# Kernel tuning notes

Hardware: AMD Instinct MI355X
Metric: run time of the kernel (lower is better)

Reference implementation:

```python
import jax, jax.numpy as jnp
import numpy as np

V, R, A, C, T = 50000, 5, 8, 32, 32  # vertices, radial, angular, in-channels, templates
DELTA = 2                             # rotation_delta -> n_rotations = A // DELTA = 4


def setup_inputs() -> dict:
    key = jax.random.key(0)
    ks = jax.random.split(key, 6)
    signal = jax.random.normal(ks[0], (V, C), jnp.float32)
    bc_idx = jax.random.randint(ks[1], (V, R, A, 3), 0, V, dtype=jnp.int32)
    w = jax.random.uniform(ks[2], (V, R, A, 3), jnp.float32)
    bc_w = w / jnp.sum(w, axis=-1, keepdims=True)  # barycentric weights sum to 1
    templ1 = jax.random.normal(ks[3], (T, R, A, C), jnp.float32) * 0.05
    bias1 = jnp.zeros((T,), jnp.float32)
    templ2 = jax.random.normal(ks[4], (T, R, A, T), jnp.float32) * 0.05
    bias2 = jnp.zeros((T,), jnp.float32)
    return {"signal": signal, "bc_idx": bc_idx, "bc_w": bc_w,
            "templ1": templ1, "bias1": bias1, "templ2": templ2, "bias2": bias2}


def _conv_dirac(x, bc_idx, bc_w, templ, bias):
    """Dirac intrinsic surface convolution.
    x: [V, Cin]; bc_idx/bc_w: [V, R, A, 3]; templ: [T, R, A, Cin] -> [V, n_rot, T]."""
    # Barycentric interpolation of the mesh signal at template vertices.
    gathered = x[bc_idx]                                   # [V, R, A, 3, Cin]
    interp = jnp.einsum('vrai,vraic->vrac', bc_w, gathered)  # [V, R, A, Cin]
    n_rot = A // DELTA
    # Rotating the patch by +s angular steps == correlating with templ rolled by +s.
    rot_t = jnp.stack([jnp.roll(templ, r * DELTA, axis=2) for r in range(n_rot)])  # [n_rot, T, R, A, Cin]
    return jnp.einsum('vrac,ntrac->vnt', interp, rot_t) + bias  # [V, n_rot, T]


def _amp(x):
    # AngularMaxPooling: max over the rotation axis.
    return jnp.max(x, axis=1)


def reference(signal, bc_idx, bc_w, templ1, bias1, templ2, bias2):
    s = jax.nn.relu(_conv_dirac(signal, bc_idx, bc_w, templ1, bias1))  # conv1 (relu)
    s = _amp(s)                                                        # [V, T]
    s = _conv_dirac(s, bc_idx, bc_w, templ2, bias2)                    # conv2 (linear)
    s = _amp(s)                                                        # [V, T]
    # input_dim == amt_templates -> no rescale branch; residual add + output relu
    return jax.nn.relu(s + signal)
```

## Files before the change

### kernel.cpp

```cpp
#include <hip/hip_runtime.h>
#include <hip/hip_bf16.h>

#define VN 50000
#define RN 5
#define AN 8
#define CN 32
#define KSTEPS 40
#define NB 8

typedef __attribute__((ext_vector_type(8))) short bf16x8;
typedef __attribute__((ext_vector_type(4))) float f32x4;
typedef __attribute__((ext_vector_type(2))) float f32x2;
typedef __attribute__((ext_vector_type(2))) int   i32x2;

__device__ __forceinline__ float b2f(short s) {
    union { unsigned u; float f; } cv;
    cv.u = ((unsigned)(unsigned short)s) << 16;
    return cv.f;
}
__device__ __forceinline__ short f2b(float f) {
    union { float f; unsigned u; } cv; cv.f = f;
    unsigned r = cv.u + 0x7fff + ((cv.u >> 16) & 1);
    return (short)(r >> 16);
}

__global__ void pack_x(const float* __restrict__ x, __hip_bfloat16* __restrict__ xb, int n4) {
    int i = blockIdx.x * blockDim.x + threadIdx.x;
    if (i >= n4) return;
    float4 v = ((const float4*)x)[i];
    ushort4 o;
    o.x = (unsigned short)f2b(v.x);
    o.y = (unsigned short)f2b(v.y);
    o.z = (unsigned short)f2b(v.z);
    o.w = (unsigned short)f2b(v.w);
    ((ushort4*)xb)[i] = o;
}

__global__ void build_Bp(const float* __restrict__ t1, const float* __restrict__ t2,
                         __hip_bfloat16* __restrict__ B1, __hip_bfloat16* __restrict__ B2) {
    int m = blockIdx.x * blockDim.x + threadIdx.x;
    if (m >= KSTEPS * NB * 64 * 8) return;
    int j = m & 7;
    int lane = (m >> 3) & 63;
    int nb = (m >> 9) & 7;
    int kstep = m >> 12;
    int c = ((lane >> 4) << 3) + j;
    int r = kstep >> 3, a = kstep & 7;
    int nt = nb * 16 + (lane & 15);
    int n = nt >> 5, t = nt & 31;
    int asrc = (a - 2 * n + 8) & 7;
    int src = ((t * RN + r) * AN + asrc) * CN + c;
    ((unsigned short*)B1)[m] = (unsigned short)f2b(t1[src]);
    ((unsigned short*)B2)[m] = (unsigned short)f2b(t2[src]);
}

template<bool FIRST>
__global__ __launch_bounds__(64, 2)
void conv_mfma(const __hip_bfloat16* __restrict__ xb,
               const int*   __restrict__ bc_idx,
               const float* __restrict__ bc_w,
               const __hip_bfloat16* __restrict__ Bp,
               const float* __restrict__ bias,
               const float* __restrict__ signal,
               __hip_bfloat16* __restrict__ out_bf,
               float* __restrict__ out_f)
{
    const int lane = threadIdx.x;
    const int vbase = blockIdx.x * 32;
    const int arow = lane & 15;
    const int c0 = (lane >> 4) << 3;

    int v0 = vbase + arow;   int vc0 = v0 < VN ? v0 : VN - 1;
    int v1 = v0 + 16;        int vc1 = v1 < VN ? v1 : VN - 1;

    const int*   ip0 = bc_idx + (size_t)vc0 * 120;
    const int*   ip1 = bc_idx + (size_t)vc1 * 120;
    const float* wp0 = bc_w   + (size_t)vc0 * 120;
    const float* wp1 = bc_w   + (size_t)vc1 * 120;
    const unsigned short* xs = (const unsigned short*)xb;
    const bf16x8* Bfrag = (const bf16x8*)Bp + lane;

    f32x4 acc[2][NB];
#pragma unroll
    for (int mi = 0; mi < 2; ++mi)
#pragma unroll
        for (int nb = 0; nb < NB; ++nb) acc[mi][nb] = (f32x4)(0.f);

    i32x2 I[3][6];
    f32x2 W[3][6];
    bf16x8 G[3][6];

    auto LOADIW = [&](int s, int p) {
        const int off = (p >> 2) * 24 + (p & 3) * 6;
#pragma unroll
        for (int q = 0; q < 3; ++q) {
            I[s][q]     = __builtin_nontemporal_load((const i32x2*)(ip0 + off) + q);
            I[s][3 + q] = __builtin_nontemporal_load((const i32x2*)(ip1 + off) + q);
            W[s][q]     = __builtin_nontemporal_load((const f32x2*)(wp0 + off) + q);
            W[s][3 + q] = __builtin_nontemporal_load((const f32x2*)(wp1 + off) + q);
        }
    };
    auto ISSUEG = [&](int g, int t) {
        const int s = (t >> 1) % 3, h = t & 1;
#pragma unroll
        for (int row = 0; row < 2; ++row)
#pragma unroll
            for (int i = 0; i < 3; ++i) {
                const int e = 3 * h + i;
                int idx = I[s][row * 3 + (e >> 1)][e & 1];
                G[g][row * 3 + i] = *(const bf16x8*)(xs + (size_t)idx * CN + c0);
            }
    };
    auto CONSUME = [&](int g, int t) {
        const int s = (t >> 1) % 3, h = t & 1;
        bf16x8 af[2];
#pragma unroll
        for (int row = 0; row < 2; ++row) {
            float w[3];
#pragma unroll
            for (int i = 0; i < 3; ++i) {
                const int e = 3 * h + i;
                w[i] = W[s][row * 3 + (e >> 1)][e & 1];
            }
#pragma unroll
            for (int j = 0; j < 8; ++j) {
                float f = fmaf(w[0], b2f(G[g][row * 3 + 0][j]),
                         fmaf(w[1], b2f(G[g][row * 3 + 1][j]),
                               w[2] * b2f(G[g][row * 3 + 2][j])));
                af[row][j] = f2b(f);
            }
        }
#pragma unroll
        for (int nb = 0; nb < NB; ++nb) {
            bf16x8 bfr = Bfrag[(t * NB + nb) * 64];
            acc[0][nb] = __builtin_amdgcn_mfma_f32_16x16x32_bf16(af[0], bfr, acc[0][nb], 0, 0, 0);
            acc[1][nb] = __builtin_amdgcn_mfma_f32_16x16x32_bf16(af[1], bfr, acc[1][nb], 0, 0, 0);
        }
    };

    LOADIW(0, 0); LOADIW(1, 1); LOADIW(2, 2);
    ISSUEG(0, 0); ISSUEG(1, 1);
#pragma unroll
    for (int t = 0; t < KSTEPS; ++t) {
        if (t + 2 < KSTEPS) ISSUEG((t + 2) % 3, t + 2);
        CONSUME(t % 3, t);
        if ((t & 1) && ((t >> 1) + 3) < 20) LOADIW(((t >> 1) + 3) % 3, (t >> 1) + 3);
    }

    const int colD = lane & 15;
    const int rbase = (lane >> 4) << 2;
#pragma unroll
    for (int mi = 0; mi < 2; ++mi) {
#pragma unroll
        for (int q = 0; q < 2; ++q) {
            f32x4 mx;
#pragma unroll
            for (int rg = 0; rg < 4; ++rg)
                mx[rg] = fmaxf(fmaxf(acc[mi][q][rg], acc[mi][q + 2][rg]),
                               fmaxf(acc[mi][q + 4][rg], acc[mi][q + 6][rg]));
            int t = q * 16 + colD;
            float b = bias[t];
#pragma unroll
            for (int rg = 0; rg < 4; ++rg) {
                int vv = vbase + mi * 16 + rbase + rg;
                if (vv < VN) {
                    float val = mx[rg] + b;
                    if (FIRST) {
                        ((unsigned short*)out_bf)[vv * CN + t] =
                            (unsigned short)f2b(fmaxf(val, 0.f));
                    } else {
                        val += __builtin_nontemporal_load(signal + vv * CN + t);
                        __builtin_nontemporal_store(fmaxf(val, 0.f), out_f + vv * CN + t);
                    }
                }
            }
        }
    }
}

extern "C" void kernel_launch(void* const* d_in, const int* in_sizes, int n_in,
                              void* d_out, int out_size, void* d_ws, size_t ws_size,
                              hipStream_t stream) {
    const float* signal = (const float*)d_in[0];
    const int*   bc_idx = (const int*)d_in[1];
    const float* bc_w   = (const float*)d_in[2];
    const float* t1     = (const float*)d_in[3];
    const float* b1     = (const float*)d_in[4];
    const float* t2     = (const float*)d_in[5];
    const float* b2     = (const float*)d_in[6];
    float* out = (float*)d_out;

    __hip_bfloat16* ws = (__hip_bfloat16*)d_ws;
    __hip_bfloat16* xb  = ws;
    __hip_bfloat16* s1  = ws + VN * CN;
    __hip_bfloat16* Bp1 = ws + 2 * VN * CN;
    __hip_bfloat16* Bp2 = Bp1 + KSTEPS * NB * 64 * 8;

    pack_x<<<(VN * CN / 4 + 255) / 256, 256, 0, stream>>>(signal, xb, VN * CN / 4);
    build_Bp<<<(KSTEPS * NB * 64 * 8) / 256, 256, 0, stream>>>(t1, t2, Bp1, Bp2);

    int blocks = (VN + 31) / 32;
    conv_mfma<true ><<<blocks, 64, 0, stream>>>(xb, bc_idx, bc_w, Bp1, b1, nullptr, s1, nullptr);
    conv_mfma<false><<<blocks, 64, 0, stream>>>(s1, bc_idx, bc_w, Bp2, b2, signal, nullptr, out);
}
```

Measured before the change: 250.6 us.

## Split K dimension across four waves per block with LDS reduction

Each 32-vertex block now runs four waves instead of one. Each wave handles a quarter of the angular K-steps (two angles per radial ring), and the partial accumulators are summed through shared memory in a two-stage tree reduction before the epilogue. The aim is more parallelism and latency hiding for the gather-heavy loop, and it replaces the hand-built three-stage software pipeline. In exchange it adds 32KB of LDS per block, three barriers, and reduction traffic, and it drops the explicit prefetch pipelining.

```diff
diff --git a/kernel.cpp b/kernel.cpp
--- a/kernel.cpp
+++ b/kernel.cpp
@@ -55,7 +55,7 @@
 }
 
 template<bool FIRST>
-__global__ __launch_bounds__(64, 2)
+__global__ __launch_bounds__(256)
 void conv_mfma(const __hip_bfloat16* __restrict__ xb,
                const int*   __restrict__ bc_idx,
                const float* __restrict__ bc_w,
@@ -65,7 +65,9 @@
                __hip_bfloat16* __restrict__ out_bf,
                float* __restrict__ out_f)
 {
-    const int lane = threadIdx.x;
+    const int tid = threadIdx.x;
+    const int wid = tid >> 6;
+    const int lane = tid & 63;
     const int vbase = blockIdx.x * 32;
     const int arow = lane & 15;
     const int c0 = (lane >> 4) << 3;
@@ -86,66 +88,76 @@
 #pragma unroll
         for (int nb = 0; nb < NB; ++nb) acc[mi][nb] = (f32x4)(0.f);
 
-    i32x2 I[3][6];
-    f32x2 W[3][6];
-    bf16x8 G[3][6];
-
-    auto LOADIW = [&](int s, int p) {
-        const int off = (p >> 2) * 24 + (p & 3) * 6;
+#pragma unroll
+    for (int r = 0; r < RN; ++r) {
+        const int off = r * 24 + wid * 6;
+        i32x2 ia[3], ib[3]; f32x2 wa[3], wb[3];
 #pragma unroll
         for (int q = 0; q < 3; ++q) {
-            I[s][q]     = __builtin_nontemporal_load((const i32x2*)(ip0 + off) + q);
-            I[s][3 + q] = __builtin_nontemporal_load((const i32x2*)(ip1 + off) + q);
-            W[s][q]     = __builtin_nontemporal_load((const f32x2*)(wp0 + off) + q);
-            W[s][3 + q] = __builtin_nontemporal_load((const f32x2*)(wp1 + off) + q);
+            ia[q] = __builtin_nontemporal_load((const i32x2*)(ip0 + off) + q);
+            ib[q] = __builtin_nontemporal_load((const i32x2*)(ip1 + off) + q);
+            wa[q] = __builtin_nontemporal_load((const f32x2*)(wp0 + off) + q);
+            wb[q] = __builtin_nontemporal_load((const f32x2*)(wp1 + off) + q);
         }
-    };
-    auto ISSUEG = [&](int g, int t) {
-        const int s = (t >> 1) % 3, h = t & 1;
-#pragma unroll
-        for (int row = 0; row < 2; ++row)
-#pragma unroll
-            for (int i = 0; i < 3; ++i) {
-                const int e = 3 * h + i;
-                int idx = I[s][row * 3 + (e >> 1)][e & 1];
-                G[g][row * 3 + i] = *(const bf16x8*)(xs + (size_t)idx * CN + c0);
+#pragma unroll
+        for (int h = 0; h < 2; ++h) {
+            bf16x8 g0a = *(const bf16x8*)(xs + (size_t)ia[(3*h+0)>>1][(3*h+0)&1] * CN + c0);
+            bf16x8 g1a = *(const bf16x8*)(xs + (size_t)ia[(3*h+1)>>1][(3*h+1)&1] * CN + c0);
+            bf16x8 g2a = *(const bf16x8*)(xs + (size_t)ia[(3*h+2)>>1][(3*h+2)&1] * CN + c0);
+            bf16x8 g0b = *(const bf16x8*)(xs + (size_t)ib[(3*h+0)>>1][(3*h+0)&1] * CN + c0);
+            bf16x8 g1b = *(const bf16x8*)(xs + (size_t)ib[(3*h+1)>>1][(3*h+1)&1] * CN + c0);
+            bf16x8 g2b = *(const bf16x8*)(xs + (size_t)ib[(3*h+2)>>1][(3*h+2)&1] * CN + c0);
+            float w0a = wa[(3*h+0)>>1][(3*h+0)&1], w1a = wa[(3*h+1)>>1][(3*h+1)&1], w2a = wa[(3*h+2)>>1][(3*h+2)&1];
+            float w0b = wb[(3*h+0)>>1][(3*h+0)&1], w1b = wb[(3*h+1)>>1][(3*h+1)&1], w2b = wb[(3*h+2)>>1][(3*h+2)&1];
+            bf16x8 af0, af1;
+#pragma unroll
+            for (int j = 0; j < 8; ++j) {
+                float fa = fmaf(w0a, b2f(g0a[j]), fmaf(w1a, b2f(g1a[j]), w2a * b2f(g2a[j])));
+                float fb = fmaf(w0b, b2f(g0b[j]), fmaf(w1b, b2f(g1b[j]), w2b * b2f(g2b[j])));
+                af0[j] = f2b(fa);
+                af1[j] = f2b(fb);
             }
-    };
-    auto CONSUME = [&](int g, int t) {
-        const int s = (t >> 1) % 3, h = t & 1;
-        bf16x8 af[2];
-#pragma unroll
-        for (int row = 0; row < 2; ++row) {
-            float w[3];
-#pragma unroll
-            for (int i = 0; i < 3; ++i) {
-                const int e = 3 * h + i;
-                w[i] = W[s][row * 3 + (e >> 1)][e & 1];
-            }
-#pragma unroll
-            for (int j = 0; j < 8; ++j) {
-                float f = fmaf(w[0], b2f(G[g][row * 3 + 0][j]),
-                         fmaf(w[1], b2f(G[g][row * 3 + 1][j]),
-                               w[2] * b2f(G[g][row * 3 + 2][j])));
-                af[row][j] = f2b(f);
+            const int ks = r * AN + 2 * wid + h;
+#pragma unroll
+            for (int nb = 0; nb < NB; ++nb) {
+                bf16x8 bfr = Bfrag[(ks * NB + nb) * 64];
+                acc[0][nb] = __builtin_amdgcn_mfma_f32_16x16x32_bf16(af0, bfr, acc[0][nb], 0, 0, 0);
+                acc[1][nb] = __builtin_amdgcn_mfma_f32_16x16x32_bf16(af1, bfr, acc[1][nb], 0, 0, 0);
             }
         }
-#pragma unroll
-        for (int nb = 0; nb < NB; ++nb) {
-            bf16x8 bfr = Bfrag[(t * NB + nb) * 64];
-            acc[0][nb] = __builtin_amdgcn_mfma_f32_16x16x32_bf16(af[0], bfr, acc[0][nb], 0, 0, 0);
-            acc[1][nb] = __builtin_amdgcn_mfma_f32_16x16x32_bf16(af[1], bfr, acc[1][nb], 0, 0, 0);
-        }
-    };
-
-    LOADIW(0, 0); LOADIW(1, 1); LOADIW(2, 2);
-    ISSUEG(0, 0); ISSUEG(1, 1);
-#pragma unroll
-    for (int t = 0; t < KSTEPS; ++t) {
-        if (t + 2 < KSTEPS) ISSUEG((t + 2) % 3, t + 2);
-        CONSUME(t % 3, t);
-        if ((t & 1) && ((t >> 1) + 3) < 20) LOADIW(((t >> 1) + 3) % 3, (t >> 1) + 3);
-    }
+    }
+
+    __shared__ f32x4 red[2][16][64];
+    if (wid >= 2) {
+#pragma unroll
+        for (int mi = 0; mi < 2; ++mi)
+#pragma unroll
+            for (int nb = 0; nb < NB; ++nb)
+                red[wid - 2][mi * 8 + nb][lane] = acc[mi][nb];
+    }
+    __syncthreads();
+    if (wid < 2) {
+#pragma unroll
+        for (int mi = 0; mi < 2; ++mi)
+#pragma unroll
+            for (int nb = 0; nb < NB; ++nb)
+                acc[mi][nb] += red[wid][mi * 8 + nb][lane];
+    }
+    __syncthreads();
+    if (wid == 1) {
+#pragma unroll
+        for (int mi = 0; mi < 2; ++mi)
+#pragma unroll
+            for (int nb = 0; nb < NB; ++nb)
+                red[0][mi * 8 + nb][lane] = acc[mi][nb];
+    }
+    __syncthreads();
+    if (wid != 0) return;
+#pragma unroll
+    for (int mi = 0; mi < 2; ++mi)
+#pragma unroll
+        for (int nb = 0; nb < NB; ++nb)
+            acc[mi][nb] += red[0][mi * 8 + nb][lane];
 
     const int colD = lane & 15;
     const int rbase = (lane >> 4) << 2;
@@ -200,6 +212,6 @@
     build_Bp<<<(KSTEPS * NB * 64 * 8) / 256, 256, 0, stream>>>(t1, t2, Bp1, Bp2);
 
     int blocks = (VN + 31) / 32;
-    conv_mfma<true ><<<blocks, 64, 0, stream>>>(xb, bc_idx, bc_w, Bp1, b1, nullptr, s1, nullptr);
-    conv_mfma<false><<<blocks, 64, 0, stream>>>(s1, bc_idx, bc_w, Bp2, b2, signal, nullptr, out);
-}
+    conv_mfma<true ><<<blocks, 256, 0, stream>>>(xb, bc_idx, bc_w, Bp1, b1, nullptr, s1, nullptr);
+    conv_mfma<false><<<blocks, 256, 0, stream>>>(s1, bc_idx, bc_w, Bp2, b2, signal, nullptr, out);
+}
```

Measured after the change: 267.0 us. 1.07x slower.
